# Kernel tuning notes

Measured on AMD Instinct MI355X. Metric: run time of the kernel, lower is better.

Reference implementation:

```python
import jax, jax.numpy as jnp
import numpy as np

H, W = 4096, 4096
KH, KW = 11, 11


def setup_inputs() -> dict:
    key = jax.random.key(0)
    k1, k2 = jax.random.split(key)
    x = jax.random.normal(k1, (H, W), dtype=jnp.float32)
    weight = jax.random.uniform(k2, (KH, KW), dtype=jnp.float32)
    bias = jnp.zeros((1,), dtype=jnp.float32)
    return {"x": x, "weight": weight, "bias": bias}


def reference(x, weight, bias):
    # corr2d: valid 2D cross-correlation of a single-channel image with a
    # single kernel, then add scalar bias. Output shape [H-KH+1, W-KW+1].
    out = jax.lax.conv_general_dilated(
        x[None, None, :, :],            # NCHW, N=C=1
        weight[None, None, :, :],       # OIHW, O=I=1
        window_strides=(1, 1),
        padding="VALID",
        dimension_numbers=("NCHW", "OIHW", "NCHW"),
    )[0, 0]
    return out + bias[0]
```

## Files before the change

### kernel.cpp

```cpp
#include <hip/hip_runtime.h>
#include <hip/hip_bf16.h>

#define IH 4096
#define IW 4096
#define KH 11
#define KW 11
#define OH (IH - KH + 1)
#define OW (IW - KW + 1)

#define BM 64
#define BN 64
#define TROWS   74
#define TCOLS   80
#define TSTRIDE 84
#define NC4     20
#define NCHUNK  (TROWS * NC4)
#define NITER   6
#define B_OFF   (TROWS * TSTRIDE)

typedef short bf16x4 __attribute__((ext_vector_type(4)));
typedef short bf16x8 __attribute__((ext_vector_type(8)));
typedef float f32x4  __attribute__((ext_vector_type(4)));

__device__ __forceinline__ short f2b(float f) {
    __hip_bfloat16 h = __float2bfloat16(f);
    return __builtin_bit_cast(short, h);
}

__global__ __launch_bounds__(256)
void conv2d_mfma(const float* __restrict__ x,
                 const float* __restrict__ w,
                 const float* __restrict__ bias,
                 float* __restrict__ out) {
    __shared__ short lds[B_OFF + KH * 512];

    const int tid = threadIdx.x;
    const int gx0 = blockIdx.x * BN;
    const int gy0 = blockIdx.y * BM;

#pragma unroll
    for (int it = 0; it < NITER; ++it) {
        const int i = tid + it * 256;
        if (i < NCHUNK) {
            const int r  = i / NC4;
            const int c4 = i - r * NC4;
            const int gy = gy0 + r;
            const int gx = gx0 + c4 * 4;
            float4 v = make_float4(0.f, 0.f, 0.f, 0.f);
            if (gy < IH && gx + 3 < IW) {
                v = *reinterpret_cast<const float4*>(x + (size_t)gy * IW + gx);
            }
            bf16x4 b = { f2b(v.x), f2b(v.y), f2b(v.z), f2b(v.w) };
            *reinterpret_cast<bf16x4*>(&lds[r * TSTRIDE + c4 * 4]) = b;
        }
    }

#pragma unroll
    for (int t = 0; t < 22; ++t) {
        const int idx = tid + t * 256;
        const int kh = idx >> 9;
        const int j  = (idx >> 5) & 15;
        const int k  = idx & 31;
        const int d  = k - j;
        const float val = (d >= 0 && d < KW) ? w[kh * KW + d] : 0.f;
        lds[B_OFF + idx] = f2b(val);
    }
    __syncthreads();

    const int lane = tid & 63;
    const int wv   = tid >> 6;
    const int g    = lane >> 4;
    const int li   = lane & 15;

    f32x4 acc[4] = {};

    const short* ap = &lds[(16 * wv + li) * TSTRIDE + g * 8];
    const short* bp = &lds[B_OFF + li * 32 + g * 8];

#pragma unroll 1
    for (int kh = 0; kh < KH; ++kh) {
        const bf16x8 bfrag = *reinterpret_cast<const bf16x8*>(bp + kh * 512);
#pragma unroll
        for (int c = 0; c < 4; ++c) {
            bf16x4 lo = *reinterpret_cast<const bf16x4*>(ap + c * 16);
            bf16x4 hi = *reinterpret_cast<const bf16x4*>(ap + c * 16 + 4);
            bf16x8 a  = __builtin_shufflevector(lo, hi, 0, 1, 2, 3, 4, 5, 6, 7);
            acc[c] = __builtin_amdgcn_mfma_f32_16x16x32_bf16(a, bfrag, acc[c],
                                                             0, 0, 0);
        }
        ap += TSTRIDE;
    }

    const float bv = bias[0];
#pragma unroll
    for (int c = 0; c < 4; ++c) {
        const int ox = gx0 + c * 16 + li;
        if (ox < OW) {
#pragma unroll
            for (int r = 0; r < 4; ++r) {
                const int oy = gy0 + wv * 16 + g * 4 + r;
                if (oy < OH) {
                    out[(size_t)oy * OW + ox] = acc[c][r] + bv;
                }
            }
        }
    }
}

extern "C" void kernel_launch(void* const* d_in, const int* in_sizes, int n_in,
                              void* d_out, int out_size, void* d_ws, size_t ws_size,
                              hipStream_t stream) {
    const float* x    = (const float*)d_in[0];
    const float* w    = (const float*)d_in[1];
    const float* bias = (const float*)d_in[2];
    float* out        = (float*)d_out;

    dim3 grid(64, 64);
    dim3 block(256);
    conv2d_mfma<<<grid, block, 0, stream>>>(x, w, bias, out);
}
```

Measured before the change: 46.11 us.

## Process two horizontal tiles per block with prefetch of second tile during compute

Each block now handles two adjacent 64x64 output tiles. The second tile's global loads are issued into registers before the first tile is computed, so load latency can overlap the MFMA work; the weight-matrix LDS setup is also shared between the two tiles. Block IDs are remapped to a 1D grid with an 8-way interleave, which changes which tiles are resident at the same time. The cost is more registers per thread (24 extra floats held live), half as many blocks for latency hiding, and extra syncthreads.

Measured after the change: 42.75 us. 7.3% less time.

```diff
diff --git a/kernel.cpp b/kernel.cpp
--- a/kernel.cpp
+++ b/kernel.cpp
@@ -11,12 +11,14 @@
 #define BM 64
 #define BN 64
 #define TROWS   74
-#define TCOLS   80
 #define TSTRIDE 84
 #define NC4     20
 #define NCHUNK  (TROWS * NC4)
 #define NITER   6
 #define B_OFF   (TROWS * TSTRIDE)
+
+#define TILES_X 64
+#define NPAIR   2048
 
 typedef short bf16x4 __attribute__((ext_vector_type(4)));
 typedef short bf16x8 __attribute__((ext_vector_type(8)));
@@ -27,53 +29,45 @@
     return __builtin_bit_cast(short, h);
 }
 
-__global__ __launch_bounds__(256)
-void conv2d_mfma(const float* __restrict__ x,
-                 const float* __restrict__ w,
-                 const float* __restrict__ bias,
-                 float* __restrict__ out) {
-    __shared__ short lds[B_OFF + KH * 512];
+__device__ __forceinline__ void stage_load(float4 G[NITER],
+                                           const float* __restrict__ x,
+                                           int gx0, int gy0, int tid) {
+#pragma unroll
+    for (int it = 0; it < NITER; ++it) {
+        const int i = tid + it * 256;
+        float4 v = make_float4(0.f, 0.f, 0.f, 0.f);
+        if (i < NCHUNK) {
+            const int r  = i / NC4;
+            const int c4 = i - r * NC4;
+            const int gy = gy0 + r;
+            const int gx = gx0 + c4 * 4;
+            if (gy < IH && gx + 3 < IW) {
+                v = *reinterpret_cast<const float4*>(x + (size_t)gy * IW + gx);
+            }
+        }
+        G[it] = v;
+    }
+}
 
-    const int tid = threadIdx.x;
-    const int gx0 = blockIdx.x * BN;
-    const int gy0 = blockIdx.y * BM;
-
+__device__ __forceinline__ void stage_write(short* __restrict__ lds,
+                                            const float4 G[NITER], int tid) {
 #pragma unroll
     for (int it = 0; it < NITER; ++it) {
         const int i = tid + it * 256;
         if (i < NCHUNK) {
             const int r  = i / NC4;
             const int c4 = i - r * NC4;
-            const int gy = gy0 + r;
-            const int gx = gx0 + c4 * 4;
-            float4 v = make_float4(0.f, 0.f, 0.f, 0.f);
-            if (gy < IH && gx + 3 < IW) {
-                v = *reinterpret_cast<const float4*>(x + (size_t)gy * IW + gx);
-            }
-            bf16x4 b = { f2b(v.x), f2b(v.y), f2b(v.z), f2b(v.w) };
+            bf16x4 b = { f2b(G[it].x), f2b(G[it].y), f2b(G[it].z), f2b(G[it].w) };
             *reinterpret_cast<bf16x4*>(&lds[r * TSTRIDE + c4 * 4]) = b;
         }
     }
+}
 
-#pragma unroll
-    for (int t = 0; t < 22; ++t) {
-        const int idx = tid + t * 256;
-        const int kh = idx >> 9;
-        const int j  = (idx >> 5) & 15;
-        const int k  = idx & 31;
-        const int d  = k - j;
-        const float val = (d >= 0 && d < KW) ? w[kh * KW + d] : 0.f;
-        lds[B_OFF + idx] = f2b(val);
-    }
-    __syncthreads();
-
-    const int lane = tid & 63;
-    const int wv   = tid >> 6;
-    const int g    = lane >> 4;
-    const int li   = lane & 15;
-
+__device__ __forceinline__ void compute_tile(const short* __restrict__ lds,
+                                             float bv, float* __restrict__ out,
+                                             int gx0, int gy0,
+                                             int wv, int g, int li) {
     f32x4 acc[4] = {};
-
     const short* ap = &lds[(16 * wv + li) * TSTRIDE + g * 8];
     const short* bp = &lds[B_OFF + li * 32 + g * 8];
 
@@ -91,7 +85,6 @@
         ap += TSTRIDE;
     }
 
-    const float bv = bias[0];
 #pragma unroll
     for (int c = 0; c < 4; ++c) {
         const int ox = gx0 + c * 16 + li;
@@ -107,6 +100,56 @@
     }
 }
 
+__global__ __launch_bounds__(256)
+void conv2d_mfma2(const float* __restrict__ x,
+                  const float* __restrict__ w,
+                  const float* __restrict__ bias,
+                  float* __restrict__ out) {
+    __shared__ short lds[B_OFF + KH * 512];
+
+    const int tid = threadIdx.x;
+    const int pair = (blockIdx.x & 7) * (NPAIR / 8) + (blockIdx.x >> 3);
+    const int t0 = pair * 2;
+    const int gy0   = (t0 >> 6) * BM;
+    const int gx0_0 = (t0 & (TILES_X - 1)) * BN;
+    const int gx0_1 = gx0_0 + BN;
+
+    const int lane = tid & 63;
+    const int wv   = tid >> 6;
+    const int g    = lane >> 4;
+    const int li   = lane & 15;
+    const float bv = bias[0];
+
+    {
+        float4 G0[NITER];
+        stage_load(G0, x, gx0_0, gy0, tid);
+        stage_write(lds, G0, tid);
+    }
+#pragma unroll
+    for (int t = 0; t < 22; ++t) {
+        const int idx = tid + t * 256;
+        const int kh = idx >> 9;
+        const int j  = (idx >> 5) & 15;
+        const int k  = idx & 31;
+        const int d  = k - j;
+        const float val = (d >= 0 && d < KW) ? w[kh * KW + d] : 0.f;
+        lds[B_OFF + idx] = f2b(val);
+    }
+    __syncthreads();
+
+    float4 G[NITER];
+    stage_load(G, x, gx0_1, gy0, tid);
+    __builtin_amdgcn_sched_barrier(0);
+
+    compute_tile(lds, bv, out, gx0_0, gy0, wv, g, li);
+
+    __syncthreads();
+    stage_write(lds, G, tid);
+    __syncthreads();
+
+    compute_tile(lds, bv, out, gx0_1, gy0, wv, g, li);
+}
+
 extern "C" void kernel_launch(void* const* d_in, const int* in_sizes, int n_in,
                               void* d_out, int out_size, void* d_ws, size_t ws_size,
                               hipStream_t stream) {
@@ -115,7 +158,7 @@
     const float* bias = (const float*)d_in[2];
     float* out        = (float*)d_out;
 
-    dim3 grid(64, 64);
+    dim3 grid(NPAIR);
     dim3 block(256);
-    conv2d_mfma<<<grid, block, 0, stream>>>(x, w, bias, out);
+    conv2d_mfma2<<<grid, block, 0, stream>>>(x, w, bias, out);
 }
```

## Split into precomputed banded weight matrix and single-wave 16-row tile blocks

Applied to the files above, without the earlier changes.

Builds the banded bf16 weight matrix once in a small prologue kernel written to workspace, instead of every block rebuilding it in LDS. The main kernel now uses one 64-thread wave per block covering a 16x64 output tile. It keeps all 11 B fragments in registers, double-buffers A fragments with fully unrolled MFMA steps, and remaps block IDs across 8 interleaved groups. The goal is to cut per-block LDS setup and barriers and raise occupancy. In exchange, overlapping input halo rows are reloaded more often (26 rows per 16 output rows instead of 74 per 64), which adds global traffic, and there is an extra kernel launch.

New measurement: 44.37 us. 3.8% less time.

```diff
diff --git a/kernel.cpp b/kernel.cpp
--- a/kernel.cpp
+++ b/kernel.cpp
@@ -8,15 +8,15 @@
 #define OH (IH - KH + 1)
 #define OW (IW - KW + 1)
 
-#define BM 64
-#define BN 64
-#define TROWS   74
-#define TCOLS   80
+#define SROWS   26
 #define TSTRIDE 84
-#define NC4     20
-#define NCHUNK  (TROWS * NC4)
-#define NITER   6
-#define B_OFF   (TROWS * TSTRIDE)
+#define NCHW    20
+#define WCHUNK  (SROWS * NCHW)
+#define TILE_SHORTS (SROWS * TSTRIDE)
+
+#define STRIPS_X 64
+#define ROWS_Y   256
+#define NBLK     (STRIPS_X * ROWS_Y)
 
 typedef short bf16x4 __attribute__((ext_vector_type(4)));
 typedef short bf16x8 __attribute__((ext_vector_type(8)));
@@ -27,34 +27,8 @@
     return __builtin_bit_cast(short, h);
 }
 
-__global__ __launch_bounds__(256)
-void conv2d_mfma(const float* __restrict__ x,
-                 const float* __restrict__ w,
-                 const float* __restrict__ bias,
-                 float* __restrict__ out) {
-    __shared__ short lds[B_OFF + KH * 512];
-
+__global__ void build_bmat(const float* __restrict__ w, short* __restrict__ bm) {
     const int tid = threadIdx.x;
-    const int gx0 = blockIdx.x * BN;
-    const int gy0 = blockIdx.y * BM;
-
-#pragma unroll
-    for (int it = 0; it < NITER; ++it) {
-        const int i = tid + it * 256;
-        if (i < NCHUNK) {
-            const int r  = i / NC4;
-            const int c4 = i - r * NC4;
-            const int gy = gy0 + r;
-            const int gx = gx0 + c4 * 4;
-            float4 v = make_float4(0.f, 0.f, 0.f, 0.f);
-            if (gy < IH && gx + 3 < IW) {
-                v = *reinterpret_cast<const float4*>(x + (size_t)gy * IW + gx);
-            }
-            bf16x4 b = { f2b(v.x), f2b(v.y), f2b(v.z), f2b(v.w) };
-            *reinterpret_cast<bf16x4*>(&lds[r * TSTRIDE + c4 * 4]) = b;
-        }
-    }
-
 #pragma unroll
     for (int t = 0; t < 22; ++t) {
         const int idx = tid + t * 256;
@@ -63,33 +37,83 @@
         const int k  = idx & 31;
         const int d  = k - j;
         const float val = (d >= 0 && d < KW) ? w[kh * KW + d] : 0.f;
-        lds[B_OFF + idx] = f2b(val);
+        bm[idx] = f2b(val);
     }
-    __syncthreads();
+}
 
-    const int lane = tid & 63;
-    const int wv   = tid >> 6;
+__global__ __launch_bounds__(64)
+void conv2d_1w(const float* __restrict__ x,
+               const short* __restrict__ bg,
+               const float* __restrict__ bias,
+               float* __restrict__ out) {
+    __shared__ short tile[TILE_SHORTS];
+
+    const int lane = threadIdx.x;
     const int g    = lane >> 4;
     const int li   = lane & 15;
 
+    const int id    = (blockIdx.x & 7) * (NBLK / 8) + (blockIdx.x >> 3);
+    const int strip = id >> 8;
+    const int ty    = id & 255;
+    const int gx0   = strip * 64;
+    const int gy0   = ty * 16;
+
+    const short* bp = bg + li * 32 + g * 8;
+#define BLOAD(KH) const bf16x8 B##KH = *reinterpret_cast<const bf16x8*>(bp + (KH) * 512)
+    BLOAD(0); BLOAD(1); BLOAD(2); BLOAD(3); BLOAD(4); BLOAD(5);
+    BLOAD(6); BLOAD(7); BLOAD(8); BLOAD(9); BLOAD(10);
+#undef BLOAD
+
+#pragma unroll
+    for (int it = 0; it < 9; ++it) {
+        const int i = lane + it * 64;
+        if (i < WCHUNK) {
+            const int r  = i / NCHW;
+            const int c4 = i - r * NCHW;
+            const int gy = gy0 + r;
+            const int gx = gx0 + c4 * 4;
+            float4 v = make_float4(0.f, 0.f, 0.f, 0.f);
+            if (gy < IH && gx + 3 < IW) {
+                v = *reinterpret_cast<const float4*>(x + (size_t)gy * IW + gx);
+            }
+            bf16x4 b = { f2b(v.x), f2b(v.y), f2b(v.z), f2b(v.w) };
+            *reinterpret_cast<bf16x4*>(&tile[r * TSTRIDE + c4 * 4]) = b;
+        }
+    }
+
     f32x4 acc[4] = {};
+    const short* ap = &tile[li * TSTRIDE + g * 8];
 
-    const short* ap = &lds[(16 * wv + li) * TSTRIDE + g * 8];
-    const short* bp = &lds[B_OFF + li * 32 + g * 8];
+    bf16x8 Ae[4], Ao[4];
+#define LOADA(A, ROW) do {                                                   \
+        const short* p_ = ap + (ROW) * TSTRIDE;                              \
+        _Pragma("unroll")                                                    \
+        for (int c = 0; c < 4; ++c) {                                        \
+            bf16x4 lo = *reinterpret_cast<const bf16x4*>(p_ + c * 16);       \
+            bf16x4 hi = *reinterpret_cast<const bf16x4*>(p_ + c * 16 + 4);   \
+            A[c] = __builtin_shufflevector(lo, hi, 0, 1, 2, 3, 4, 5, 6, 7);  \
+        }                                                                    \
+    } while (0)
+#define MFMA4(A, B) do {                                                     \
+        _Pragma("unroll")                                                    \
+        for (int c = 0; c < 4; ++c)                                          \
+            acc[c] = __builtin_amdgcn_mfma_f32_16x16x32_bf16(A[c], B,        \
+                                                             acc[c], 0, 0, 0); \
+    } while (0)
+#define STEPE(KH, B) LOADA(Ao, (KH) + 1); MFMA4(Ae, B); \
+        __builtin_amdgcn_sched_barrier(0)
+#define STEPO(KH, B) LOADA(Ae, (KH) + 1); MFMA4(Ao, B); \
+        __builtin_amdgcn_sched_barrier(0)
 
-#pragma unroll 1
-    for (int kh = 0; kh < KH; ++kh) {
-        const bf16x8 bfrag = *reinterpret_cast<const bf16x8*>(bp + kh * 512);
-#pragma unroll
-        for (int c = 0; c < 4; ++c) {
-            bf16x4 lo = *reinterpret_cast<const bf16x4*>(ap + c * 16);
-            bf16x4 hi = *reinterpret_cast<const bf16x4*>(ap + c * 16 + 4);
-            bf16x8 a  = __builtin_shufflevector(lo, hi, 0, 1, 2, 3, 4, 5, 6, 7);
-            acc[c] = __builtin_amdgcn_mfma_f32_16x16x32_bf16(a, bfrag, acc[c],
-                                                             0, 0, 0);
-        }
-        ap += TSTRIDE;
-    }
+    LOADA(Ae, 0);
+    STEPE(0, B0);  STEPO(1, B1);  STEPE(2, B2);  STEPO(3, B3);
+    STEPE(4, B4);  STEPO(5, B5);  STEPE(6, B6);  STEPO(7, B7);
+    STEPE(8, B8);  STEPO(9, B9);  MFMA4(Ae, B10);
+
+#undef STEPE
+#undef STEPO
+#undef MFMA4
+#undef LOADA
 
     const float bv = bias[0];
 #pragma unroll
@@ -98,7 +122,7 @@
         if (ox < OW) {
 #pragma unroll
             for (int r = 0; r < 4; ++r) {
-                const int oy = gy0 + wv * 16 + g * 4 + r;
+                const int oy = gy0 + g * 4 + r;
                 if (oy < OH) {
                     out[(size_t)oy * OW + ox] = acc[c][r] + bv;
                 }
@@ -114,8 +138,11 @@
     const float* w    = (const float*)d_in[1];
     const float* bias = (const float*)d_in[2];
     float* out        = (float*)d_out;
+    short* bm         = (short*)d_ws;
 
-    dim3 grid(64, 64);
-    dim3 block(256);
-    conv2d_mfma<<<grid, block, 0, stream>>>(x, w, bias, out);
+    build_bmat<<<dim3(1), dim3(256), 0, stream>>>(w, bm);
+
+    dim3 grid(NBLK);
+    dim3 block(64);
+    conv2d_1w<<<grid, block, 0, stream>>>(x, bm, bias, out);
 }
```
